# Performance work log

Measured on AMD Instinct MI355X. Metric: run time of the kernel, lower is better.

## Reference

```python
import jax, jax.numpy as jnp
import numpy as np

N = 100000
E = 800000
IN_DIM = 256
H = 4
C = 32          # per-head hidden dim
SLOPE = 0.2


def gat_conv(x, W, att_src, att_dst, bias, src, dst):
    """PyG GATConv (single input tensor => lin_src applied to both src and dst),
    concat=True, add_self_loops=False, eval mode (no attn dropout).
    x: [N, F_in], W: [H*C, F_in], att_src/att_dst: [H, C], bias: [H*C].
    Returns [N, H*C]."""
    n = x.shape[0]
    xp = (x @ W.T).reshape(n, H, C)                    # [N,H,C]
    a_src = jnp.einsum('nhc,hc->nh', xp, att_src)      # [N,H]
    a_dst = jnp.einsum('nhc,hc->nh', xp, att_dst)      # [N,H]
    e = a_src[src] + a_dst[dst]                        # [E,H]
    e = jax.nn.leaky_relu(e, SLOPE)
    # segment softmax over incoming edges of each dst node
    m = jax.ops.segment_max(e, dst, num_segments=n)    # [N,H]
    ex = jnp.exp(e - m[dst])                           # [E,H]
    s = jax.ops.segment_sum(ex, dst, num_segments=n)   # [N,H]
    alpha = ex / (s[dst] + 1e-16)                      # [E,H]
    msg = xp[src] * alpha[:, :, None]                  # [E,H,C]
    out = jax.ops.segment_sum(msg, dst, num_segments=n)  # [N,H,C]
    return out.reshape(n, H * C) + bias


def setup_inputs() -> dict:
    key = jax.random.key(0)
    ks = jax.random.split(key, 12)
    x = jax.random.normal(ks[0], (N, IN_DIM), dtype=jnp.float32)
    edge_index = jax.random.randint(ks[1], (2, E), 0, N, dtype=jnp.int64)
    g = 1.414

    def xavier(k, shape):
        fan_in, fan_out = shape[-1], int(np.prod(shape[:-1]))
        std = g * np.sqrt(2.0 / (fan_in + fan_out))
        return jax.random.normal(k, shape, dtype=jnp.float32) * std

    W0 = xavier(ks[2], (H * C, IN_DIM))
    att_src0 = xavier(ks[3], (H, C))
    att_dst0 = xavier(ks[4], (H, C))
    b0 = jnp.zeros((H * C,), dtype=jnp.float32)
    W1 = xavier(ks[5], (H * C, H * C))
    att_src1 = xavier(ks[6], (H, C))
    att_dst1 = xavier(ks[7], (H, C))
    b1 = jnp.zeros((H * C,), dtype=jnp.float32)
    return {"x": x, "edge_index": edge_index,
            "W0": W0, "att_src0": att_src0, "att_dst0": att_dst0, "b0": b0,
            "W1": W1, "att_src1": att_src1, "att_dst1": att_dst1, "b1": b1}


def reference(x, edge_index, W0, att_src0, att_dst0, b0, W1, att_src1, att_dst1, b1):
    src, dst = edge_index[0], edge_index[1]
    h = gat_conv(x, W0, att_src0, att_dst0, b0, src, dst)
    h = jax.nn.relu(h)                 # activation on all but last layer
    h = gat_conv(h, W1, att_src1, att_dst1, b1, src, dst)
    # encoding=False => no last activation; head is Identity
    return h
```

## Files before the change

### kernel.cpp

```cpp
#include <hip/hip_runtime.h>
#include <hip/hip_bf16.h>
#include <cstdint>
#include <cstddef>
#include <type_traits>

#define SLOPE 0.2f

typedef __attribute__((ext_vector_type(8))) short short8v;
typedef __attribute__((ext_vector_type(4))) float float4v;

__device__ inline ushort f2bf(float f) {
  uint u = __float_as_uint(f);
  uint r = (u + 0x7FFFu + ((u >> 16) & 1u)) >> 16;
  return (ushort)r;
}
__device__ inline float bf2f(ushort u) {
  return __uint_as_float(((uint)u) << 16);
}
__device__ inline float bflo(uint u) { return __uint_as_float(u << 16); }
__device__ inline float bfhi(uint u) { return __uint_as_float(u & 0xffff0000u); }

__device__ inline short8v pack8(float4 a, float4 b) {
  uint4 r;
  r.x = (uint)f2bf(a.x) | ((uint)f2bf(a.y) << 16);
  r.y = (uint)f2bf(a.z) | ((uint)f2bf(a.w) << 16);
  r.z = (uint)f2bf(b.x) | ((uint)f2bf(b.y) << 16);
  r.w = (uint)f2bf(b.z) | ((uint)f2bf(b.w) << 16);
  return __builtin_bit_cast(short8v, r);
}
__device__ inline float lrelu(float v) { return (v > 0.f) ? v : SLOPE * v; }


__global__ void k_init(const float* __restrict__ W0, const float* __restrict__ W1,
                       ushort* __restrict__ Wb0, ushort* __restrict__ Wb1,
                       int4* __restrict__ counts4, int n4) {
  int i = blockIdx.x * 256 + threadIdx.x;
  if (i < 128 * 256) Wb0[i] = f2bf(W0[i]);
  if (i < 128 * 128) Wb1[i] = f2bf(W1[i]);
  if (i < n4) counts4[i] = make_int4(0, 0, 0, 0);
}


__global__ void k_count(const int* __restrict__ dst, int* __restrict__ counts, int E) {
  int e = blockIdx.x * 256 + threadIdx.x;
  if (e < E) atomicAdd(&counts[dst[e]], 1);
}

__global__ void k_scan1(const int* __restrict__ counts, int* __restrict__ excl,
                        int* __restrict__ bsums, int N) {
  __shared__ int lds[256];
  int tid = threadIdx.x;
  int base = blockIdx.x * 2048 + tid * 8;
  int v[8];
  int ts = 0;
#pragma unroll
  for (int i = 0; i < 8; i++) {
    int idx = base + i;
    int t = (idx < N) ? counts[idx] : 0;
    v[i] = ts;
    ts += t;
  }
  lds[tid] = ts;
  __syncthreads();
  for (int off = 1; off < 256; off <<= 1) {
    int t = (tid >= off) ? lds[tid - off] : 0;
    __syncthreads();
    lds[tid] += t;
    __syncthreads();
  }
  int texcl = (tid > 0) ? lds[tid - 1] : 0;
#pragma unroll
  for (int i = 0; i < 8; i++) {
    int idx = base + i;
    if (idx < N) excl[idx] = texcl + v[i];
  }
  if (tid == 255) bsums[blockIdx.x] = lds[255];
}

__global__ void k_scan2(int* bsums, int nb) {
  __shared__ int lds[256];
  int tid = threadIdx.x;
  int v = (tid < nb) ? bsums[tid] : 0;
  lds[tid] = v;
  __syncthreads();
  for (int off = 1; off < 256; off <<= 1) {
    int t = (tid >= off) ? lds[tid - off] : 0;
    __syncthreads();
    lds[tid] += t;
    __syncthreads();
  }
  if (tid < nb) bsums[tid] = (tid > 0) ? lds[tid - 1] : 0;
}

__global__ void k_scan3(int* __restrict__ excl, int* __restrict__ cursor,
                        const int* __restrict__ bsums, int N) {
  int tid = threadIdx.x;
  int off = bsums[blockIdx.x];
  int base = blockIdx.x * 2048 + tid * 8;
#pragma unroll
  for (int i = 0; i < 8; i++) {
    int idx = base + i;
    if (idx < N) {
      int val = excl[idx] + off;
      excl[idx] = val;
      cursor[idx] = val;
    }
  }
}

__global__ void k_fill(const int* __restrict__ src, const int* __restrict__ dst,
                       int* __restrict__ cursor, int* __restrict__ src_sorted, int E) {
  int e = blockIdx.x * 256 + threadIdx.x;
  if (e < E) {
    int d = dst[e];
    int pos = atomicAdd(&cursor[d], 1);
    src_sorted[pos] = src[e];
  }
}


template <typename AT, int K>
__global__ __launch_bounds__(256, 4) void k_gemm_lds(
    const AT* __restrict__ A, const ushort* __restrict__ Wb,
    const float* __restrict__ att_src, const float* __restrict__ att_dst,
    ushort* __restrict__ C, float* __restrict__ a_src, float* __restrict__ a_dst,
    int M) {
  constexpr int KH = 128;
  constexpr int LDW = KH + 8;
  __shared__ ushort Ws[128 * LDW];
  const int tid = threadIdx.x;
  const int wave = tid >> 6, lane = tid & 63;
  const int fr = lane & 15, fq = lane >> 4;
  const int bm = blockIdx.x * 64;
  const int r0 = bm + wave * 16 + fr;
  const int rc0 = min(r0, M - 1);
  const AT* arow = A + (size_t)rc0 * K + fq * 8;

  const int sr = tid >> 1;
  const int scb = (tid & 1) * (KH / 2);
  const ushort* wrow = Wb + (size_t)sr * K + scb;
  ushort* drow = &Ws[sr * LDW + scb];

#pragma unroll
  for (int i = 0; i < KH / 16; i++)
    *(uint4*)(drow + i * 8) = *(const uint4*)(wrow + i * 8);

  float4v acc[8] = {};

  if constexpr (std::is_same<AT, float>::value) {
    float4 a0[4][2];
#pragma unroll
    for (int s = 0; s < 4; s++) {
      const float* p = arow + s * 32;
      a0[s][0] = *(const float4*)p;
      a0[s][1] = *(const float4*)(p + 4);
    }
    __syncthreads();
#pragma unroll
    for (int s = 0; s < 4; s++) {
      short8v af = pack8(a0[s][0], a0[s][1]);
#pragma unroll
      for (int t = 0; t < 8; t++) {
        short8v bfr = *(const short8v*)&Ws[(t * 16 + fr) * LDW + s * 32 + fq * 8];
        acc[t] = __builtin_amdgcn_mfma_f32_16x16x32_bf16(af, bfr, acc[t], 0, 0, 0);
      }
    }
    float4 a1[4][2];
#pragma unroll
    for (int s = 0; s < 4; s++) {
      const float* p = arow + KH + s * 32;
      a1[s][0] = *(const float4*)p;
      a1[s][1] = *(const float4*)(p + 4);
    }
    __syncthreads();
#pragma unroll
    for (int i = 0; i < KH / 16; i++)
      *(uint4*)(drow + i * 8) = *(const uint4*)(wrow + KH + i * 8);
    __syncthreads();
#pragma unroll
    for (int s = 0; s < 4; s++) {
      short8v af = pack8(a1[s][0], a1[s][1]);
#pragma unroll
      for (int t = 0; t < 8; t++) {
        short8v bfr = *(const short8v*)&Ws[(t * 16 + fr) * LDW + s * 32 + fq * 8];
        acc[t] = __builtin_amdgcn_mfma_f32_16x16x32_bf16(af, bfr, acc[t], 0, 0, 0);
      }
    }
  } else {
    short8v a0[4];
#pragma unroll
    for (int s = 0; s < 4; s++)
      a0[s] = *(const short8v*)(arow + s * 32);
    __syncthreads();
#pragma unroll
    for (int s = 0; s < 4; s++) {
#pragma unroll
      for (int t = 0; t < 8; t++) {
        short8v bfr = *(const short8v*)&Ws[(t * 16 + fr) * LDW + s * 32 + fq * 8];
        acc[t] = __builtin_amdgcn_mfma_f32_16x16x32_bf16(a0[s], bfr, acc[t], 0, 0, 0);
      }
    }
  }

  float asc[8], adc[8];
#pragma unroll
  for (int t = 0; t < 8; t++) {
    asc[t] = att_src[t * 16 + fr];
    adc[t] = att_dst[t * 16 + fr];
  }

#pragma unroll
  for (int j = 0; j < 4; j++) {
    int row = bm + wave * 16 + fq * 4 + j;
    bool ok = row < M;
    if (ok) {
#pragma unroll
      for (int t = 0; t < 8; t++)
        C[(size_t)row * 128 + t * 16 + fr] = f2bf(acc[t][j]);
    }
    float ps[4], pd[4];
#pragma unroll
    for (int h = 0; h < 4; h++) {
      ps[h] = acc[2 * h][j] * asc[2 * h] + acc[2 * h + 1][j] * asc[2 * h + 1];
      pd[h] = acc[2 * h][j] * adc[2 * h] + acc[2 * h + 1][j] * adc[2 * h + 1];
    }
#pragma unroll
    for (int off = 1; off < 16; off <<= 1) {
#pragma unroll
      for (int h = 0; h < 4; h++) {
        ps[h] += __shfl_xor(ps[h], off);
        pd[h] += __shfl_xor(pd[h], off);
      }
    }
    if (ok && fr == 0) {
      *(float4*)&a_src[(size_t)row * 4] = make_float4(ps[0], ps[1], ps[2], ps[3]);
      *(float4*)&a_dst[(size_t)row * 4] = make_float4(pd[0], pd[1], pd[2], pd[3]);
    }
  }
}


template <bool RELU, typename OT>
__global__ __launch_bounds__(256) void k_agg(const ushort* __restrict__ xp,
                                             const float* __restrict__ a_src,
                                             const float* __restrict__ a_dst,
                                             const int* __restrict__ src_sorted,
                                             const int* __restrict__ indptr,
                                             const int* __restrict__ counts,
                                             const float* __restrict__ bias,
                                             OT* __restrict__ out, int N) {
  int tid = threadIdx.x;
  int n = blockIdx.x * 8 + (tid >> 5);
  if (n >= N) return;
  int c4 = tid & 31;
  int h = c4 >> 3;
  int deg = counts[n];
  int start = indptr[n];
  const int* sp = src_sorted + start;
  const ushort* xpc = xp + c4 * 4;
  const float* asrc_h = a_src + h;
  float ad = a_dst[(size_t)n * 4 + h];

  float a0 = 0.f, a1 = 0.f, a2 = 0.f, a3 = 0.f, s = 0.f;
  int i = 0;
  for (; i + 4 <= deg; i += 4) {
    int s0 = sp[i], s1 = sp[i + 1], s2 = sp[i + 2], s3 = sp[i + 3];
    float e0 = asrc_h[(size_t)s0 * 4], e1 = asrc_h[(size_t)s1 * 4];
    float e2 = asrc_h[(size_t)s2 * 4], e3 = asrc_h[(size_t)s3 * 4];
    uint2 v0 = *(const uint2*)(xpc + (size_t)s0 * 128);
    uint2 v1 = *(const uint2*)(xpc + (size_t)s1 * 128);
    uint2 v2 = *(const uint2*)(xpc + (size_t)s2 * 128);
    uint2 v3 = *(const uint2*)(xpc + (size_t)s3 * 128);
    float x0 = __expf(lrelu(e0 + ad)), x1 = __expf(lrelu(e1 + ad));
    float x2 = __expf(lrelu(e2 + ad)), x3 = __expf(lrelu(e3 + ad));
    s += x0 + x1 + x2 + x3;
    a0 = fmaf(bflo(v0.x), x0, a0); a1 = fmaf(bfhi(v0.x), x0, a1);
    a2 = fmaf(bflo(v0.y), x0, a2); a3 = fmaf(bfhi(v0.y), x0, a3);
    a0 = fmaf(bflo(v1.x), x1, a0); a1 = fmaf(bfhi(v1.x), x1, a1);
    a2 = fmaf(bflo(v1.y), x1, a2); a3 = fmaf(bfhi(v1.y), x1, a3);
    a0 = fmaf(bflo(v2.x), x2, a0); a1 = fmaf(bfhi(v2.x), x2, a1);
    a2 = fmaf(bflo(v2.y), x2, a2); a3 = fmaf(bfhi(v2.y), x2, a3);
    a0 = fmaf(bflo(v3.x), x3, a0); a1 = fmaf(bfhi(v3.x), x3, a1);
    a2 = fmaf(bflo(v3.y), x3, a2); a3 = fmaf(bfhi(v3.y), x3, a3);
  }
  for (; i < deg; i++) {
    int s0 = sp[i];
    float x0 = __expf(lrelu(asrc_h[(size_t)s0 * 4] + ad));
    uint2 v0 = *(const uint2*)(xpc + (size_t)s0 * 128);
    s += x0;
    a0 = fmaf(bflo(v0.x), x0, a0); a1 = fmaf(bfhi(v0.x), x0, a1);
    a2 = fmaf(bflo(v0.y), x0, a2); a3 = fmaf(bfhi(v0.y), x0, a3);
  }

  float inv = 1.f / (s + 1e-16f);
  float4 bv = *(const float4*)&bias[c4 * 4];
  float o0 = fmaf(a0, inv, bv.x);
  float o1 = fmaf(a1, inv, bv.y);
  float o2 = fmaf(a2, inv, bv.z);
  float o3 = fmaf(a3, inv, bv.w);
  if (RELU) {
    o0 = fmaxf(o0, 0.f); o1 = fmaxf(o1, 0.f);
    o2 = fmaxf(o2, 0.f); o3 = fmaxf(o3, 0.f);
  }
  if constexpr (std::is_same<OT, float>::value) {
    *(float4*)&out[(size_t)n * 128 + c4 * 4] = make_float4(o0, o1, o2, o3);
  } else {
    uint2 pk;
    pk.x = (uint)f2bf(o0) | ((uint)f2bf(o1) << 16);
    pk.y = (uint)f2bf(o2) | ((uint)f2bf(o3) << 16);
    *(uint2*)&((ushort*)out)[(size_t)n * 128 + c4 * 4] = pk;
  }
}


extern "C" void kernel_launch(void* const* d_in, const int* in_sizes, int n_in,
                              void* d_out, int out_size, void* d_ws, size_t ws_size,
                              hipStream_t stream) {
  const float* x   = (const float*)d_in[0];
  const int*   ei  = (const int*)d_in[1];
  const float* W0  = (const float*)d_in[2];
  const float* as0 = (const float*)d_in[3];
  const float* ad0 = (const float*)d_in[4];
  const float* b0  = (const float*)d_in[5];
  const float* W1  = (const float*)d_in[6];
  const float* as1 = (const float*)d_in[7];
  const float* ad1 = (const float*)d_in[8];
  const float* b1  = (const float*)d_in[9];

  const int N = in_sizes[0] / 256;
  const int E = in_sizes[1] / 2;
  const int* src = ei;
  const int* dst = ei + E;

  char* ws = (char*)d_ws;
  size_t off = 0;
  auto alloc = [&](size_t bytes) -> void* {
    void* p = ws + off;
    off += (bytes + 255) & ~(size_t)255;
    return p;
  };
  ushort* xp    = (ushort*)alloc((size_t)N * 128 * 2);
  ushort* hbuf  = (ushort*)alloc((size_t)N * 128 * 2);
  float* a_src  = (float*)alloc((size_t)N * 4 * 4);
  float* a_dst  = (float*)alloc((size_t)N * 4 * 4);
  int*   counts = (int*)alloc((size_t)N * 4);
  int*   indptr = (int*)alloc((size_t)N * 4);
  int*   cursor = (int*)alloc((size_t)N * 4);
  int*   ssort  = (int*)alloc((size_t)E * 4);
  int*   bsums  = (int*)alloc(256 * 4);
  ushort* Wb0   = (ushort*)alloc((size_t)128 * 256 * 2);
  ushort* Wb1   = (ushort*)alloc((size_t)128 * 128 * 2);

  int n4 = N / 4;
  int eb = (E + 255) / 256;
  int nb = (N + 2047) / 2048;
  k_init<<<128, 256, 0, stream>>>(W0, W1, Wb0, Wb1, (int4*)counts, n4);
  k_count<<<eb, 256, 0, stream>>>(dst, counts, E);
  k_scan1<<<nb, 256, 0, stream>>>(counts, indptr, bsums, N);
  k_scan2<<<1, 256, 0, stream>>>(bsums, nb);
  k_scan3<<<nb, 256, 0, stream>>>(indptr, cursor, bsums, N);
  k_fill<<<eb, 256, 0, stream>>>(src, dst, cursor, ssort, E);

  int gb = (N + 63) / 64;
  int gb8 = (N + 7) / 8;

  k_gemm_lds<float, 256><<<gb, 256, 0, stream>>>(x, Wb0, as0, ad0, xp,
                                                 a_src, a_dst, N);
  k_agg<true, ushort><<<gb8, 256, 0, stream>>>(xp, a_src, a_dst, ssort, indptr,
                                               counts, b0, hbuf, N);

  k_gemm_lds<ushort, 128><<<gb, 256, 0, stream>>>(hbuf, Wb1, as1, ad1, xp,
                                                  a_src, a_dst, N);
  k_agg<false, float><<<gb8, 256, 0, stream>>>(xp, a_src, a_dst, ssort, indptr,
                                               counts, b1, (float*)d_out, N);
}
```

Baseline: 250.7 us.

## Split aggregation edges across four lane groups and merge scan kernels

The aggregation kernel now gives each destination node a full 64-lane wavefront. Lanes are split into four edge groups of 16, each lane loading 8 bf16 channels with a 16-byte load, and the partial sums are combined with cross-lane xor shuffles. This raises memory-level parallelism for the gathers when degrees are small, but adds shuffle reductions and leaves three quarters of the lanes idle during the epilogue. Separately, the scan2 and scan3 kernels are merged: each block sums the preceding block totals serially, which removes one kernel launch.

```diff
diff --git a/kernel.cpp b/kernel.cpp
--- a/kernel.cpp
+++ b/kernel.cpp
@@ -77,25 +77,11 @@
   if (tid == 255) bsums[blockIdx.x] = lds[255];
 }
 
-__global__ void k_scan2(int* bsums, int nb) {
-  __shared__ int lds[256];
+__global__ void k_scan23(int* __restrict__ excl, int* __restrict__ cursor,
+                         const int* __restrict__ bsums, int N) {
+  int off = 0;
+  for (int j = 0; j < blockIdx.x; j++) off += bsums[j];
   int tid = threadIdx.x;
-  int v = (tid < nb) ? bsums[tid] : 0;
-  lds[tid] = v;
-  __syncthreads();
-  for (int off = 1; off < 256; off <<= 1) {
-    int t = (tid >= off) ? lds[tid - off] : 0;
-    __syncthreads();
-    lds[tid] += t;
-    __syncthreads();
-  }
-  if (tid < nb) bsums[tid] = (tid > 0) ? lds[tid - 1] : 0;
-}
-
-__global__ void k_scan3(int* __restrict__ excl, int* __restrict__ cursor,
-                        const int* __restrict__ bsums, int N) {
-  int tid = threadIdx.x;
-  int off = bsums[blockIdx.x];
   int base = blockIdx.x * 2048 + tid * 8;
 #pragma unroll
   for (int i = 0; i < 8; i++) {
@@ -250,65 +236,63 @@
                                              const float* __restrict__ bias,
                                              OT* __restrict__ out, int N) {
   int tid = threadIdx.x;
-  int n = blockIdx.x * 8 + (tid >> 5);
+  int n = blockIdx.x * 4 + (tid >> 6);
   if (n >= N) return;
-  int c4 = tid & 31;
-  int h = c4 >> 3;
+  int lane = tid & 63;
+  int e4 = lane >> 4;
+  int c8 = lane & 15;
+  int h = c8 >> 2;
   int deg = counts[n];
   int start = indptr[n];
   const int* sp = src_sorted + start;
-  const ushort* xpc = xp + c4 * 4;
+  const ushort* xpc = xp + c8 * 8;
   const float* asrc_h = a_src + h;
   float ad = a_dst[(size_t)n * 4 + h];
 
-  float a0 = 0.f, a1 = 0.f, a2 = 0.f, a3 = 0.f, s = 0.f;
-  int i = 0;
-  for (; i + 4 <= deg; i += 4) {
-    int s0 = sp[i], s1 = sp[i + 1], s2 = sp[i + 2], s3 = sp[i + 3];
-    float e0 = asrc_h[(size_t)s0 * 4], e1 = asrc_h[(size_t)s1 * 4];
-    float e2 = asrc_h[(size_t)s2 * 4], e3 = asrc_h[(size_t)s3 * 4];
-    uint2 v0 = *(const uint2*)(xpc + (size_t)s0 * 128);
-    uint2 v1 = *(const uint2*)(xpc + (size_t)s1 * 128);
-    uint2 v2 = *(const uint2*)(xpc + (size_t)s2 * 128);
-    uint2 v3 = *(const uint2*)(xpc + (size_t)s3 * 128);
-    float x0 = __expf(lrelu(e0 + ad)), x1 = __expf(lrelu(e1 + ad));
-    float x2 = __expf(lrelu(e2 + ad)), x3 = __expf(lrelu(e3 + ad));
-    s += x0 + x1 + x2 + x3;
-    a0 = fmaf(bflo(v0.x), x0, a0); a1 = fmaf(bfhi(v0.x), x0, a1);
-    a2 = fmaf(bflo(v0.y), x0, a2); a3 = fmaf(bfhi(v0.y), x0, a3);
-    a0 = fmaf(bflo(v1.x), x1, a0); a1 = fmaf(bfhi(v1.x), x1, a1);
-    a2 = fmaf(bflo(v1.y), x1, a2); a3 = fmaf(bfhi(v1.y), x1, a3);
-    a0 = fmaf(bflo(v2.x), x2, a0); a1 = fmaf(bfhi(v2.x), x2, a1);
-    a2 = fmaf(bflo(v2.y), x2, a2); a3 = fmaf(bfhi(v2.y), x2, a3);
-    a0 = fmaf(bflo(v3.x), x3, a0); a1 = fmaf(bfhi(v3.x), x3, a1);
-    a2 = fmaf(bflo(v3.y), x3, a2); a3 = fmaf(bfhi(v3.y), x3, a3);
-  }
-  for (; i < deg; i++) {
-    int s0 = sp[i];
-    float x0 = __expf(lrelu(asrc_h[(size_t)s0 * 4] + ad));
-    uint2 v0 = *(const uint2*)(xpc + (size_t)s0 * 128);
-    s += x0;
-    a0 = fmaf(bflo(v0.x), x0, a0); a1 = fmaf(bfhi(v0.x), x0, a1);
-    a2 = fmaf(bflo(v0.y), x0, a2); a3 = fmaf(bfhi(v0.y), x0, a3);
-  }
-
-  float inv = 1.f / (s + 1e-16f);
-  float4 bv = *(const float4*)&bias[c4 * 4];
-  float o0 = fmaf(a0, inv, bv.x);
-  float o1 = fmaf(a1, inv, bv.y);
-  float o2 = fmaf(a2, inv, bv.z);
-  float o3 = fmaf(a3, inv, bv.w);
-  if (RELU) {
-    o0 = fmaxf(o0, 0.f); o1 = fmaxf(o1, 0.f);
-    o2 = fmaxf(o2, 0.f); o3 = fmaxf(o3, 0.f);
-  }
-  if constexpr (std::is_same<OT, float>::value) {
-    *(float4*)&out[(size_t)n * 128 + c4 * 4] = make_float4(o0, o1, o2, o3);
-  } else {
-    uint2 pk;
-    pk.x = (uint)f2bf(o0) | ((uint)f2bf(o1) << 16);
-    pk.y = (uint)f2bf(o2) | ((uint)f2bf(o3) << 16);
-    *(uint2*)&((ushort*)out)[(size_t)n * 128 + c4 * 4] = pk;
+  float a0 = 0.f, a1 = 0.f, a2 = 0.f, a3 = 0.f;
+  float a4 = 0.f, a5 = 0.f, a6 = 0.f, a7 = 0.f, s = 0.f;
+  for (int i = e4; i < deg; i += 4) {
+    int sidx = sp[i];
+    float x = __expf(lrelu(asrc_h[(size_t)sidx * 4] + ad));
+    uint4 v = *(const uint4*)(xpc + (size_t)sidx * 128);
+    s += x;
+    a0 = fmaf(bflo(v.x), x, a0); a1 = fmaf(bfhi(v.x), x, a1);
+    a2 = fmaf(bflo(v.y), x, a2); a3 = fmaf(bfhi(v.y), x, a3);
+    a4 = fmaf(bflo(v.z), x, a4); a5 = fmaf(bfhi(v.z), x, a5);
+    a6 = fmaf(bflo(v.w), x, a6); a7 = fmaf(bfhi(v.w), x, a7);
+  }
+#pragma unroll
+  for (int off = 16; off <= 32; off <<= 1) {
+    a0 += __shfl_xor(a0, off); a1 += __shfl_xor(a1, off);
+    a2 += __shfl_xor(a2, off); a3 += __shfl_xor(a3, off);
+    a4 += __shfl_xor(a4, off); a5 += __shfl_xor(a5, off);
+    a6 += __shfl_xor(a6, off); a7 += __shfl_xor(a7, off);
+    s  += __shfl_xor(s,  off);
+  }
+  if (e4 == 0) {
+    float inv = 1.f / (s + 1e-16f);
+    float4 bv0 = *(const float4*)&bias[c8 * 8];
+    float4 bv1 = *(const float4*)&bias[c8 * 8 + 4];
+    float o0 = fmaf(a0, inv, bv0.x), o1 = fmaf(a1, inv, bv0.y);
+    float o2 = fmaf(a2, inv, bv0.z), o3 = fmaf(a3, inv, bv0.w);
+    float o4 = fmaf(a4, inv, bv1.x), o5 = fmaf(a5, inv, bv1.y);
+    float o6 = fmaf(a6, inv, bv1.z), o7 = fmaf(a7, inv, bv1.w);
+    if (RELU) {
+      o0 = fmaxf(o0, 0.f); o1 = fmaxf(o1, 0.f); o2 = fmaxf(o2, 0.f);
+      o3 = fmaxf(o3, 0.f); o4 = fmaxf(o4, 0.f); o5 = fmaxf(o5, 0.f);
+      o6 = fmaxf(o6, 0.f); o7 = fmaxf(o7, 0.f);
+    }
+    if constexpr (std::is_same<OT, float>::value) {
+      *(float4*)&out[(size_t)n * 128 + c8 * 8] = make_float4(o0, o1, o2, o3);
+      *(float4*)&out[(size_t)n * 128 + c8 * 8 + 4] = make_float4(o4, o5, o6, o7);
+    } else {
+      uint4 pk;
+      pk.x = (uint)f2bf(o0) | ((uint)f2bf(o1) << 16);
+      pk.y = (uint)f2bf(o2) | ((uint)f2bf(o3) << 16);
+      pk.z = (uint)f2bf(o4) | ((uint)f2bf(o5) << 16);
+      pk.w = (uint)f2bf(o6) | ((uint)f2bf(o7) << 16);
+      *(uint4*)&((ushort*)out)[(size_t)n * 128 + c8 * 8] = pk;
+    }
   }
 }
 
@@ -357,20 +341,19 @@
   k_init<<<128, 256, 0, stream>>>(W0, W1, Wb0, Wb1, (int4*)counts, n4);
   k_count<<<eb, 256, 0, stream>>>(dst, counts, E);
   k_scan1<<<nb, 256, 0, stream>>>(counts, indptr, bsums, N);
-  k_scan2<<<1, 256, 0, stream>>>(bsums, nb);
-  k_scan3<<<nb, 256, 0, stream>>>(indptr, cursor, bsums, N);
+  k_scan23<<<nb, 256, 0, stream>>>(indptr, cursor, bsums, N);
   k_fill<<<eb, 256, 0, stream>>>(src, dst, cursor, ssort, E);
 
   int gb = (N + 63) / 64;
-  int gb8 = (N + 7) / 8;
+  int gb4 = (N + 3) / 4;
 
   k_gemm_lds<float, 256><<<gb, 256, 0, stream>>>(x, Wb0, as0, ad0, xp,
                                                  a_src, a_dst, N);
-  k_agg<true, ushort><<<gb8, 256, 0, stream>>>(xp, a_src, a_dst, ssort, indptr,
+  k_agg<true, ushort><<<gb4, 256, 0, stream>>>(xp, a_src, a_dst, ssort, indptr,
                                                counts, b0, hbuf, N);
 
   k_gemm_lds<ushort, 128><<<gb, 256, 0, stream>>>(hbuf, Wb1, as1, ad1, xp,
                                                   a_src, a_dst, N);
-  k_agg<false, float><<<gb8, 256, 0, stream>>>(xp, a_src, a_dst, ssort, indptr,
+  k_agg<false, float><<<gb4, 256, 0, stream>>>(xp, a_src, a_dst, ssort, indptr,
                                                counts, b1, (float*)d_out, N);
 }
```

After: 268.9 us. 7.2% more time.

## Precompute per-edge exp attention weights in separate kernel; merge scan passes

Applied to the files above, without the earlier changes.

Adds a k_wedge kernel that computes exp(leaky_relu(a_src+a_dst)) for all four heads per edge in CSR order and writes them to a buffer. The aggregation kernel then reads these weights instead of doing scattered a_src gathers and exps per lane. To support this, the fill step also records dst_sorted. Separately, scan2 and scan3 are merged into one kernel in which each block serially sums the preceding block totals. The trade-off is an extra E*16-byte buffer that is written and read back, plus two more launches per forward pass.

```diff
diff --git a/kernel.cpp b/kernel.cpp
--- a/kernel.cpp
+++ b/kernel.cpp
@@ -77,25 +77,11 @@
   if (tid == 255) bsums[blockIdx.x] = lds[255];
 }
 
-__global__ void k_scan2(int* bsums, int nb) {
-  __shared__ int lds[256];
+__global__ void k_scan23(int* __restrict__ excl, int* __restrict__ cursor,
+                         const int* __restrict__ bsums, int N) {
+  int off = 0;
+  for (int j = 0; j < blockIdx.x; j++) off += bsums[j];
   int tid = threadIdx.x;
-  int v = (tid < nb) ? bsums[tid] : 0;
-  lds[tid] = v;
-  __syncthreads();
-  for (int off = 1; off < 256; off <<= 1) {
-    int t = (tid >= off) ? lds[tid - off] : 0;
-    __syncthreads();
-    lds[tid] += t;
-    __syncthreads();
-  }
-  if (tid < nb) bsums[tid] = (tid > 0) ? lds[tid - 1] : 0;
-}
-
-__global__ void k_scan3(int* __restrict__ excl, int* __restrict__ cursor,
-                        const int* __restrict__ bsums, int N) {
-  int tid = threadIdx.x;
-  int off = bsums[blockIdx.x];
   int base = blockIdx.x * 2048 + tid * 8;
 #pragma unroll
   for (int i = 0; i < 8; i++) {
@@ -109,12 +95,15 @@
 }
 
 __global__ void k_fill(const int* __restrict__ src, const int* __restrict__ dst,
-                       int* __restrict__ cursor, int* __restrict__ src_sorted, int E) {
+                       int* __restrict__ cursor,
+                       int* __restrict__ src_sorted, int* __restrict__ dst_sorted,
+                       int E) {
   int e = blockIdx.x * 256 + threadIdx.x;
   if (e < E) {
     int d = dst[e];
     int pos = atomicAdd(&cursor[d], 1);
     src_sorted[pos] = src[e];
+    dst_sorted[pos] = d;
   }
 }
 
@@ -240,10 +229,26 @@
 }
 
 
+__global__ void k_wedge(const int* __restrict__ ssort, const int* __restrict__ dsort,
+                        const float* __restrict__ a_src, const float* __restrict__ a_dst,
+                        float* __restrict__ w, int E) {
+  int p = blockIdx.x * 256 + threadIdx.x;
+  if (p >= E) return;
+  int s = ssort[p], d = dsort[p];
+  float4 as4 = *(const float4*)&a_src[(size_t)s * 4];
+  float4 ad4 = *(const float4*)&a_dst[(size_t)d * 4];
+  float4 wv;
+  wv.x = __expf(lrelu(as4.x + ad4.x));
+  wv.y = __expf(lrelu(as4.y + ad4.y));
+  wv.z = __expf(lrelu(as4.z + ad4.z));
+  wv.w = __expf(lrelu(as4.w + ad4.w));
+  *(float4*)&w[(size_t)p * 4] = wv;
+}
+
+
 template <bool RELU, typename OT>
 __global__ __launch_bounds__(256) void k_agg(const ushort* __restrict__ xp,
-                                             const float* __restrict__ a_src,
-                                             const float* __restrict__ a_dst,
+                                             const float* __restrict__ wbuf,
                                              const int* __restrict__ src_sorted,
                                              const int* __restrict__ indptr,
                                              const int* __restrict__ counts,
@@ -257,22 +262,19 @@
   int deg = counts[n];
   int start = indptr[n];
   const int* sp = src_sorted + start;
+  const float* wp = wbuf + (size_t)start * 4 + h;
   const ushort* xpc = xp + c4 * 4;
-  const float* asrc_h = a_src + h;
-  float ad = a_dst[(size_t)n * 4 + h];
 
   float a0 = 0.f, a1 = 0.f, a2 = 0.f, a3 = 0.f, s = 0.f;
   int i = 0;
   for (; i + 4 <= deg; i += 4) {
     int s0 = sp[i], s1 = sp[i + 1], s2 = sp[i + 2], s3 = sp[i + 3];
-    float e0 = asrc_h[(size_t)s0 * 4], e1 = asrc_h[(size_t)s1 * 4];
-    float e2 = asrc_h[(size_t)s2 * 4], e3 = asrc_h[(size_t)s3 * 4];
+    float x0 = wp[(i + 0) * 4], x1 = wp[(i + 1) * 4];
+    float x2 = wp[(i + 2) * 4], x3 = wp[(i + 3) * 4];
     uint2 v0 = *(const uint2*)(xpc + (size_t)s0 * 128);
     uint2 v1 = *(const uint2*)(xpc + (size_t)s1 * 128);
     uint2 v2 = *(const uint2*)(xpc + (size_t)s2 * 128);
     uint2 v3 = *(const uint2*)(xpc + (size_t)s3 * 128);
-    float x0 = __expf(lrelu(e0 + ad)), x1 = __expf(lrelu(e1 + ad));
-    float x2 = __expf(lrelu(e2 + ad)), x3 = __expf(lrelu(e3 + ad));
     s += x0 + x1 + x2 + x3;
     a0 = fmaf(bflo(v0.x), x0, a0); a1 = fmaf(bfhi(v0.x), x0, a1);
     a2 = fmaf(bflo(v0.y), x0, a2); a3 = fmaf(bfhi(v0.y), x0, a3);
@@ -285,7 +287,7 @@
   }
   for (; i < deg; i++) {
     int s0 = sp[i];
-    float x0 = __expf(lrelu(asrc_h[(size_t)s0 * 4] + ad));
+    float x0 = wp[i * 4];
     uint2 v0 = *(const uint2*)(xpc + (size_t)s0 * 128);
     s += x0;
     a0 = fmaf(bflo(v0.x), x0, a0); a1 = fmaf(bfhi(v0.x), x0, a1);
@@ -343,10 +345,12 @@
   ushort* hbuf  = (ushort*)alloc((size_t)N * 128 * 2);
   float* a_src  = (float*)alloc((size_t)N * 4 * 4);
   float* a_dst  = (float*)alloc((size_t)N * 4 * 4);
+  float* wbuf   = (float*)alloc((size_t)E * 4 * 4);
   int*   counts = (int*)alloc((size_t)N * 4);
   int*   indptr = (int*)alloc((size_t)N * 4);
   int*   cursor = (int*)alloc((size_t)N * 4);
   int*   ssort  = (int*)alloc((size_t)E * 4);
+  int*   dsort  = (int*)alloc((size_t)E * 4);
   int*   bsums  = (int*)alloc(256 * 4);
   ushort* Wb0   = (ushort*)alloc((size_t)128 * 256 * 2);
   ushort* Wb1   = (ushort*)alloc((size_t)128 * 128 * 2);
@@ -357,20 +361,21 @@
   k_init<<<128, 256, 0, stream>>>(W0, W1, Wb0, Wb1, (int4*)counts, n4);
   k_count<<<eb, 256, 0, stream>>>(dst, counts, E);
   k_scan1<<<nb, 256, 0, stream>>>(counts, indptr, bsums, N);
-  k_scan2<<<1, 256, 0, stream>>>(bsums, nb);
-  k_scan3<<<nb, 256, 0, stream>>>(indptr, cursor, bsums, N);
-  k_fill<<<eb, 256, 0, stream>>>(src, dst, cursor, ssort, E);
+  k_scan23<<<nb, 256, 0, stream>>>(indptr, cursor, bsums, N);
+  k_fill<<<eb, 256, 0, stream>>>(src, dst, cursor, ssort, dsort, E);
 
   int gb = (N + 63) / 64;
   int gb8 = (N + 7) / 8;
 
   k_gemm_lds<float, 256><<<gb, 256, 0, stream>>>(x, Wb0, as0, ad0, xp,
                                                  a_src, a_dst, N);
-  k_agg<true, ushort><<<gb8, 256, 0, stream>>>(xp, a_src, a_dst, ssort, indptr,
+  k_wedge<<<eb, 256, 0, stream>>>(ssort, dsort, a_src, a_dst, wbuf, E);
+  k_agg<true, ushort><<<gb8, 256, 0, stream>>>(xp, wbuf, ssort, indptr,
                                                counts, b0, hbuf, N);
 
   k_gemm_lds<ushort, 128><<<gb, 256, 0, stream>>>(hbuf, Wb1, as1, ad1, xp,
                                                   a_src, a_dst, N);
-  k_agg<false, float><<<gb8, 256, 0, stream>>>(xp, a_src, a_dst, ssort, indptr,
+  k_wedge<<<eb, 256, 0, stream>>>(ssort, dsort, a_src, a_dst, wbuf, E);
+  k_agg<false, float><<<gb8, 256, 0, stream>>>(xp, wbuf, ssort, indptr,
                                                counts, b1, (float*)d_out, N);
 }
```

New measurement: 258.3 us. 3.0% more time.
